# Kernel optimization log

Hardware: AMD Instinct MI355X
Metric: run time of the kernel (lower is better)

## Reference

```python
import jax, jax.numpy as jnp
import numpy as np
import math

VOCAB, D, L, B, S = 32000, 1024, 6, 4, 1024
FF = 4 * D


def sinusoidal_pe(max_len, d_model):
    pos = np.arange(max_len)[:, None].astype(np.float32)
    div = np.exp(np.arange(0, d_model, 2).astype(np.float32) * (-math.log(10000.0) / d_model))
    pe = np.zeros((max_len, d_model), dtype=np.float32)
    pe[:, 0::2] = np.sin(pos * div)
    pe[:, 1::2] = np.cos(pos * div)
    return jnp.asarray(pe)


def layernorm(x, g, b, eps=1e-5):
    mu = jnp.mean(x, axis=-1, keepdims=True)
    var = jnp.mean(jnp.square(x - mu), axis=-1, keepdims=True)
    return (x - mu) * jax.lax.rsqrt(var + eps) * g + b


def setup_inputs() -> dict:
    key = jax.random.key(0)
    ks = jax.random.split(key, 16)
    s = 0.02
    inp = {
        "input_ids": jax.random.randint(ks[0], (B, S), 0, VOCAB, dtype=jnp.int32),
        "attention_mask": jnp.ones((B, S), dtype=jnp.int32),
        "emb": jax.random.normal(ks[1], (VOCAB, D), jnp.float32) * s,
        "Wq": jax.random.normal(ks[2], (L, D, D), jnp.float32) * s,
        "Wk": jax.random.normal(ks[3], (L, D, D), jnp.float32) * s,
        "Wv": jax.random.normal(ks[4], (L, D, D), jnp.float32) * s,
        "bq": jnp.zeros((L, D), jnp.float32),
        "bk": jnp.zeros((L, D), jnp.float32),
        "bv": jnp.zeros((L, D), jnp.float32),
        "g1": jnp.ones((L, D), jnp.float32),
        "beta1": jnp.zeros((L, D), jnp.float32),
        "Wf1": jax.random.normal(ks[5], (L, D, FF), jnp.float32) * s,
        "bf1": jnp.zeros((L, FF), jnp.float32),
        "Wf2": jax.random.normal(ks[6], (L, FF, D), jnp.float32) * s,
        "bf2": jnp.zeros((L, D), jnp.float32),
        "g2": jnp.ones((L, D), jnp.float32),
        "beta2": jnp.zeros((L, D), jnp.float32),
    }
    return inp


def reference(input_ids, attention_mask, emb, Wq, Wk, Wv, bq, bk, bv,
              g1, beta1, Wf1, bf1, Wf2, bf2, g2, beta2):
    pe = sinusoidal_pe(1024, D)
    x = emb[input_ids] + pe[: input_ids.shape[1]]           # [B,S,D]
    mask = (attention_mask[:, None, :] != 0)                # [B,1,S]
    scale = 1.0 / math.sqrt(D)
    for l in range(L):
        Q = jnp.einsum('bsd,de->bse', x, Wq[l]) + bq[l]
        K = jnp.einsum('bsd,de->bse', x, Wk[l]) + bk[l]
        V = jnp.einsum('bsd,de->bse', x, Wv[l]) + bv[l]
        scores = jnp.einsum('bqd,bkd->bqk', Q, K) * scale   # [B,S,S]
        scores = jnp.where(mask, scores, -1e9)
        attn = jax.nn.softmax(scores, axis=-1)
        a = jnp.einsum('bqk,bkd->bqd', attn, V)
        x = layernorm(x + a, g1[l], beta1[l])
        h = jax.nn.relu(jnp.einsum('bsd,df->bsf', x, Wf1[l]) + bf1[l])
        f = jnp.einsum('bsf,fd->bsd', h, Wf2[l]) + bf2[l]
        x = layernorm(x + f, g2[l], beta2[l])
    return x
```

## Files before the change

### kernel.cpp

```cpp
#include <hip/hip_runtime.h>

typedef __bf16 bf16_t;
typedef __bf16 bf16x8 __attribute__((ext_vector_type(8)));
typedef float f32x4 __attribute__((ext_vector_type(4)));
typedef unsigned short u16;

#define DEV static __device__ __forceinline__

DEV float bf2f(u16 u) { __bf16 h = __builtin_bit_cast(__bf16, u); return (float)h; }
DEV u16 f2bf(float f) { __bf16 h = (__bf16)f; return __builtin_bit_cast(u16, h); }

DEV void gll16(bf16_t* lds, const bf16_t* g) {
    __builtin_amdgcn_global_load_lds(
        (const __attribute__((address_space(1))) void*)g,
        (__attribute__((address_space(3))) void*)lds, 16, 0, 0);
}

#define WAITV(N) asm volatile("s_waitcnt vmcnt(" #N ")" ::: "memory")

template <int EPI>
__global__ __launch_bounds__(512, 1)
void gemm8p(const bf16_t* __restrict__ A, int lda,
            const bf16_t* __restrict__ Bt, int ldb,
            bf16_t* __restrict__ C, int ldc,
            const float* __restrict__ bias, int K,
            long kadv, long cadv)
{
    __shared__ bf16_t Asm[2 * 2 * 8192];
    __shared__ bf16_t Bsm[2 * 2 * 8192];
    const int tid = threadIdx.x, w = tid >> 6, l = tid & 63;
    const int z = blockIdx.z;
    A  += (size_t)z * kadv;
    Bt += (size_t)z * kadv;
    C  += (size_t)z * cadv;

    const int gx = gridDim.x;
    int lin = blockIdx.y * gx + blockIdx.x;
    const int nlin = gx * gridDim.y;
    lin = (lin & 7) * (nlin >> 3) + (lin >> 3);
    const size_t row0 = (size_t)(lin / gx) * 256;
    const size_t col0 = (size_t)(lin % gx) * 256;

    const int wr = w >> 2, wc = w & 3;
    const int bh = wc >> 1;
    const int browoff = (wc & 1) * 64;
    const int fr = l & 15, q = l >> 4, sw = l & 7;

    const int srow = w * 8 + (l >> 3);
    const int sslot8 = ((l & 7) ^ ((l >> 3) & 7)) * 8;
    const bf16_t* AgH0 = A  + (row0 + srow) * (size_t)lda + sslot8;
    const bf16_t* BgH0 = Bt + (col0 + srow) * (size_t)ldb + sslot8;
    const size_t a128 = (size_t)128 * lda, b128 = (size_t)128 * ldb;
    const size_t a64  = (size_t)64 * lda,  b64  = (size_t)64 * ldb;
    const int wlds = w * 512;

#define STAGE_PAIR(buf, tt, p)                                                 \
    do {                                                                       \
        const int koff = (tt) * 64;                                            \
        if ((p) == 0) {                                                        \
            gll16(Asm + ((buf)*2+0)*8192 + wlds,        AgH0 + koff);          \
            gll16(Asm + ((buf)*2+0)*8192 + 4096 + wlds, AgH0 + koff + a64);    \
        } else if ((p) == 1) {                                                 \
            gll16(Asm + ((buf)*2+1)*8192 + wlds,        AgH0 + a128 + koff);   \
            gll16(Asm + ((buf)*2+1)*8192 + 4096 + wlds, AgH0 + a128 + koff + a64); \
        } else if ((p) == 2) {                                                 \
            gll16(Bsm + ((buf)*2+0)*8192 + wlds,        BgH0 + koff);          \
            gll16(Bsm + ((buf)*2+0)*8192 + 4096 + wlds, BgH0 + koff + b64);    \
        } else {                                                               \
            gll16(Bsm + ((buf)*2+1)*8192 + wlds,        BgH0 + b128 + koff);   \
            gll16(Bsm + ((buf)*2+1)*8192 + 4096 + wlds, BgH0 + b128 + koff + b64); \
        }                                                                      \
    } while (0)

    f32x4 acc[8][4] = {};
    const int NT = K >> 6;

    STAGE_PAIR(0, 0, 0); STAGE_PAIR(0, 0, 1); STAGE_PAIR(0, 0, 2); STAGE_PAIR(0, 0, 3);
    if (NT > 1) { STAGE_PAIR(1, 1, 0); WAITV(2); } else { WAITV(0); }
    __builtin_amdgcn_sched_barrier(0);
    __builtin_amdgcn_s_barrier();

    for (int t = 0; t < NT; ++t) {
        const int cur = t & 1, nxt = cur ^ 1;
        const bool hasN1 = (t + 1 < NT), hasN2 = (t + 2 < NT);
        const bf16_t* Ab = Asm + (cur * 2 + wr) * 8192;
        const bf16_t* Bb = Bsm + (cur * 2 + bh) * 8192;

        bf16x8 aR[4][2], bR[4][2];
#pragma unroll
        for (int mi = 0; mi < 4; mi++)
#pragma unroll
            for (int kk = 0; kk < 2; kk++)
                aR[mi][kk] = *(const bf16x8*)&Ab[(mi * 16 + fr) * 64 + ((kk * 4 + q) ^ sw) * 8];
#pragma unroll
        for (int ni = 0; ni < 4; ni++)
#pragma unroll
            for (int kk = 0; kk < 2; kk++)
                bR[ni][kk] = *(const bf16x8*)&Bb[(browoff + ni * 16 + fr) * 64 + ((kk * 4 + q) ^ sw) * 8];
        if (hasN1) { STAGE_PAIR(nxt, t + 1, 1); STAGE_PAIR(nxt, t + 1, 2); }
        __builtin_amdgcn_s_setprio(1);
#pragma unroll
        for (int mi = 0; mi < 4; mi++)
#pragma unroll
            for (int ni = 0; ni < 4; ni++)
#pragma unroll
                for (int kk = 0; kk < 2; kk++)
                    acc[mi][ni] = __builtin_amdgcn_mfma_f32_16x16x32_bf16(aR[mi][kk], bR[ni][kk], acc[mi][ni], 0, 0, 0);
        __builtin_amdgcn_s_setprio(0);

        bf16x8 a2[4][2];
#pragma unroll
        for (int mi = 0; mi < 4; mi++)
#pragma unroll
            for (int kk = 0; kk < 2; kk++)
                a2[mi][kk] = *(const bf16x8*)&Ab[((4 + mi) * 16 + fr) * 64 + ((kk * 4 + q) ^ sw) * 8];
        if (hasN1) STAGE_PAIR(nxt, t + 1, 3);
        __builtin_amdgcn_s_setprio(1);
#pragma unroll
        for (int mi = 0; mi < 4; mi++)
#pragma unroll
            for (int ni = 0; ni < 4; ni++)
#pragma unroll
                for (int kk = 0; kk < 2; kk++)
                    acc[4 + mi][ni] = __builtin_amdgcn_mfma_f32_16x16x32_bf16(a2[mi][kk], bR[ni][kk], acc[4 + mi][ni], 0, 0, 0);
        __builtin_amdgcn_s_setprio(0);

        __builtin_amdgcn_s_barrier();
        if (hasN2) STAGE_PAIR(cur, t + 2, 0);
        if (hasN1) {
            if (hasN2) { WAITV(2); } else { WAITV(0); }
            __builtin_amdgcn_sched_barrier(0);
        }
        __builtin_amdgcn_s_barrier();
    }
#undef STAGE_PAIR

    const int cr = q * 4, cc = fr;
#pragma unroll
    for (int ni = 0; ni < 4; ni++) {
        size_t c = col0 + wc * 64 + ni * 16 + cc;
        float bv = bias ? bias[c] : 0.f;
#pragma unroll
        for (int mi = 0; mi < 8; mi++) {
            size_t r = row0 + wr * 128 + mi * 16 + cr;
#pragma unroll
            for (int j = 0; j < 4; j++) {
                float v = acc[mi][ni][j] + bv;
                if (EPI == 1) v = fmaxf(v, 0.f);
                C[(r + j) * ldc + c] = (bf16_t)v;
            }
        }
    }
}

template <int EPI>
__global__ __launch_bounds__(256)
void gemm_db(const bf16_t* __restrict__ A, int lda, long sA,
             const bf16_t* __restrict__ Bt, int ldb, long sB,
             void* __restrict__ Cv, int ldc, long sC,
             const float* __restrict__ bias, int K, float scale)
{
    __shared__ bf16_t Asm[2][128 * 64];
    __shared__ bf16_t Bsm[2][128 * 64];
    const int tid = threadIdx.x, w = tid >> 6, l = tid & 63;
    const int bz = blockIdx.z;

    const int gx = gridDim.x;
    int lin = blockIdx.y * gx + blockIdx.x;
    const int nlin = gx * gridDim.y;
    lin = (lin & 7) * (nlin >> 3) + (lin >> 3);
    const size_t row0 = (size_t)(lin / gx) * 128;
    const size_t col0 = (size_t)(lin % gx) * 128;

    A  += (size_t)bz * sA;
    Bt += (size_t)bz * sB;

    const int lr = l >> 3;
    const int sl = (l & 7) ^ lr;
    const bf16_t* Ag = A  + (row0 + (size_t)(w * 32) + lr) * lda + sl * 8;
    const bf16_t* Bg = Bt + (col0 + (size_t)(w * 32) + lr) * ldb + sl * 8;
    const int wlds = (w * 32) * 64;

#define STA(buf, tt)                                                           \
    do { const int ko = (tt) * 64;                                             \
        _Pragma("unroll")                                                      \
        for (int c = 0; c < 4; c++)                                            \
            gll16(&Asm[buf][wlds + c * 8 * 64], Ag + (size_t)(c * 8) * lda + ko); \
    } while (0)
#define STB(buf, tt)                                                           \
    do { const int ko = (tt) * 64;                                             \
        _Pragma("unroll")                                                      \
        for (int c = 0; c < 4; c++)                                            \
            gll16(&Bsm[buf][wlds + c * 8 * 64], Bg + (size_t)(c * 8) * ldb + ko); \
    } while (0)

    const int wm = (w >> 1) * 64, wn = (w & 1) * 64;
    const int fr16 = l & 15, q4 = l >> 4, sw = l & 7;
    f32x4 acc[4][4] = {};
    const int NT = K >> 6;

    STA(0, 0); STB(0, 0);
    if (NT > 1) { STA(1, 1); WAITV(4); } else { WAITV(0); }
    __builtin_amdgcn_sched_barrier(0);
    __builtin_amdgcn_s_barrier();

    for (int t = 0; t < NT; ++t) {
        const int cur = t & 1, nxt = cur ^ 1;
        const bool hasN1 = (t + 1 < NT), hasN2 = (t + 2 < NT);

        bf16x8 a0[4], b0[4], a1[4], b1[4];
        const int s0 = (q4 ^ sw) * 8, s1 = ((4 + q4) ^ sw) * 8;
#pragma unroll
        for (int i = 0; i < 4; i++) {
            a0[i] = *(const bf16x8*)&Asm[cur][(wm + i * 16 + fr16) * 64 + s0];
            b0[i] = *(const bf16x8*)&Bsm[cur][(wn + i * 16 + fr16) * 64 + s0];
        }
        if (hasN1) STB(nxt, t + 1);
        __builtin_amdgcn_s_setprio(1);
#pragma unroll
        for (int mi = 0; mi < 4; mi++)
#pragma unroll
            for (int ni = 0; ni < 4; ni++)
                acc[mi][ni] = __builtin_amdgcn_mfma_f32_16x16x32_bf16(a0[mi], b0[ni], acc[mi][ni], 0, 0, 0);
        __builtin_amdgcn_s_setprio(0);
#pragma unroll
        for (int i = 0; i < 4; i++) {
            a1[i] = *(const bf16x8*)&Asm[cur][(wm + i * 16 + fr16) * 64 + s1];
            b1[i] = *(const bf16x8*)&Bsm[cur][(wn + i * 16 + fr16) * 64 + s1];
        }
        __builtin_amdgcn_s_setprio(1);
#pragma unroll
        for (int mi = 0; mi < 4; mi++)
#pragma unroll
            for (int ni = 0; ni < 4; ni++)
                acc[mi][ni] = __builtin_amdgcn_mfma_f32_16x16x32_bf16(a1[mi], b1[ni], acc[mi][ni], 0, 0, 0);
        __builtin_amdgcn_s_setprio(0);

        __builtin_amdgcn_s_barrier();
        if (hasN2) STA(cur, t + 2);
        if (hasN1) {
            if (hasN2) { WAITV(4); } else { WAITV(0); }
            __builtin_amdgcn_sched_barrier(0);
        }
        __builtin_amdgcn_s_barrier();
    }
#undef STA
#undef STB

    const int cr = q4 * 4, cc = fr16;
    if (EPI == 2) {
        float* C = (float*)Cv + (size_t)bz * sC;
#pragma unroll
        for (int mi = 0; mi < 4; mi++)
#pragma unroll
            for (int ni = 0; ni < 4; ni++) {
                size_t r = row0 + wm + mi * 16 + cr;
                size_t c = col0 + wn + ni * 16 + cc;
#pragma unroll
                for (int j = 0; j < 4; j++)
                    C[(r + j) * ldc + c] = acc[mi][ni][j] * scale;
            }
    } else if (EPI == 3) {
        bf16_t* C = (bf16_t*)Cv + (size_t)bz * sC;
#pragma unroll
        for (int mi = 0; mi < 4; mi++)
#pragma unroll
            for (int ni = 0; ni < 4; ni++) {
                size_t r = row0 + wm + mi * 16 + cr;
                size_t c = col0 + wn + ni * 16 + cc;
#pragma unroll
                for (int j = 0; j < 4; j++)
                    C[(r + j) * ldc + c] = (bf16_t)(acc[mi][ni][j] * scale);
            }
    } else {
        bf16_t* C = (bf16_t*)Cv + (size_t)bz * sC;
#pragma unroll
        for (int ni = 0; ni < 4; ni++) {
            size_t c = col0 + wn + ni * 16 + cc;
            float bv = bias ? bias[c] : 0.f;
#pragma unroll
            for (int mi = 0; mi < 4; mi++) {
                size_t r = row0 + wm + mi * 16 + cr;
#pragma unroll
                for (int j = 0; j < 4; j++) {
                    float v = acc[mi][ni][j] + bv;
                    if (EPI == 1) v = fmaxf(v, 0.f);
                    C[(r + j) * ldc + c] = (bf16_t)v;
                }
            }
        }
    }
}

__global__ __launch_bounds__(256)
void prep_kernel(const float* __restrict__ Wq, const float* __restrict__ Wk,
                 const float* __restrict__ Wv, const float* __restrict__ Wf1,
                 const float* __restrict__ Wf2,
                 const float* __restrict__ bq, const float* __restrict__ bk,
                 const float* __restrict__ bv,
                 const int* __restrict__ ids, const float* __restrict__ emb,
                 bf16_t* __restrict__ wqkvTA, bf16_t* __restrict__ wf1TA,
                 bf16_t* __restrict__ wf2TA, float* __restrict__ qbiasA,
                 float* __restrict__ x, bf16_t* __restrict__ xb)
{
    __shared__ bf16_t tls[64 * 64];
    const size_t DD = 1024 * 1024;
    int id = blockIdx.x;
    if (id < 16896) {
        const float* src; bf16_t* dst; int ldin, ldout, bx, by;
        if (id < 4608) {
            int layer = id / 768, r = id % 768, which = r >> 8, t = r & 255;
            src = (which == 0 ? Wq : which == 1 ? Wk : Wv) + (size_t)layer * DD;
            dst = wqkvTA + (size_t)layer * 3 * DD + (size_t)which * DD;
            ldin = 1024; ldout = 1024; bx = (t & 15) * 64; by = (t >> 4) * 64;
        } else if (id < 10752) {
            int i = id - 4608, layer = i >> 10, t = i & 1023;
            src = Wf1 + (size_t)layer * 4 * DD; dst = wf1TA + (size_t)layer * 4 * DD;
            ldin = 4096; ldout = 1024; bx = (t & 63) * 64; by = (t >> 6) * 64;
        } else {
            int i = id - 10752, layer = i >> 10, t = i & 1023;
            src = Wf2 + (size_t)layer * 4 * DD; dst = wf2TA + (size_t)layer * 4 * DD;
            ldin = 1024; ldout = 4096; bx = (t & 15) * 64; by = (t >> 4) * 64;
        }
        const int tid = threadIdx.x;
        const int cg = tid & 15, ri = tid >> 4;
#pragma unroll
        for (int k = 0; k < 4; k++) {
            int r = ri + k * 16;
            float4 v = *(const float4*)&src[(size_t)(by + r) * ldin + bx + cg * 4];
            ushort4 o = {f2bf(v.x), f2bf(v.y), f2bf(v.z), f2bf(v.w)};
            int g = cg ^ ((r >> 2) & 15);
            *(ushort4*)&tls[r * 64 + g * 4] = o;
        }
        __syncthreads();
#pragma unroll
        for (int k = 0; k < 4; k++) {
            int i2 = ri + k * 16;
            int gr = (i2 >> 2) ^ cg;
            ushort4 o;
            o.x = __builtin_bit_cast(u16, tls[(cg * 4 + 0) * 64 + gr * 4 + (i2 & 3)]);
            o.y = __builtin_bit_cast(u16, tls[(cg * 4 + 1) * 64 + gr * 4 + (i2 & 3)]);
            o.z = __builtin_bit_cast(u16, tls[(cg * 4 + 2) * 64 + gr * 4 + (i2 & 3)]);
            o.w = __builtin_bit_cast(u16, tls[(cg * 4 + 3) * 64 + gr * 4 + (i2 & 3)]);
            *(ushort4*)&dst[(size_t)(bx + i2) * ldout + by + cg * 4] = o;
        }
        return;
    }
    id -= 16896;
    if (id < 72) {
        int i = id * 256 + threadIdx.x;
        int lyr = i / 3072, j = i - lyr * 3072;
        qbiasA[i] = (j < 1024) ? bq[lyr * 1024 + j]
                  : (j < 2048) ? bk[lyr * 1024 + j - 1024]
                               : bv[lyr * 1024 + j - 2048];
        return;
    }
    id -= 72;
    const int row = id;
    const int s = row & 1023;
    const int eid = ids[row];
    const float* er = emb + (size_t)eid * 1024;
    float* xr = x + (size_t)row * 1024;
    bf16_t* br = xb + (size_t)row * 1024;
#pragma unroll
    for (int k = 0; k < 2; k++) {
        int i = threadIdx.x + 256 * k;
        int d = 2 * i;
        float dv = expf((float)d * -0.008994473019508f);
        float ph = (float)s * dv;
        float sv, cv;
        sincosf(ph, &sv, &cv);
        float2 ev = *(const float2*)&er[d];
        float x0 = ev.x + sv;
        float x1 = ev.y + cv;
        float2 xo = {x0, x1};
        *(float2*)&xr[d] = xo;
        ushort2 bo = {f2bf(x0), f2bf(x1)};
        *(ushort2*)&br[d] = bo;
    }
}

__global__ __launch_bounds__(256)
void softvt_kernel(const bf16_t* __restrict__ sc, const int* __restrict__ amask,
                   bf16_t* __restrict__ p, const bf16_t* __restrict__ qkv,
                   bf16_t* __restrict__ vt)
{
    __shared__ bf16_t tls[64][72];
    int bid = blockIdx.x;
    if (bid < 1024) {
        const int row = bid * 4 + (threadIdx.x >> 6);
        const int l = threadIdx.x & 63;
        const int b = row >> 10;
        const bf16_t* s = sc + (size_t)row * 1024;
        const int* m = amask + (size_t)b * 1024;
        float v[16];
        float mx = -3.0e38f;
#pragma unroll
        for (int i = 0; i < 4; i++) {
            int c = 4 * l + 256 * i;
            ushort4 su = *(const ushort4*)&s[c];
            int4 mv = *(const int4*)&m[c];
            v[4 * i + 0] = mv.x ? bf2f(su.x) : -1e9f;
            v[4 * i + 1] = mv.y ? bf2f(su.y) : -1e9f;
            v[4 * i + 2] = mv.z ? bf2f(su.z) : -1e9f;
            v[4 * i + 3] = mv.w ? bf2f(su.w) : -1e9f;
            mx = fmaxf(mx, fmaxf(fmaxf(v[4 * i], v[4 * i + 1]), fmaxf(v[4 * i + 2], v[4 * i + 3])));
        }
#pragma unroll
        for (int o = 32; o; o >>= 1) mx = fmaxf(mx, __shfl_xor(mx, o, 64));
        float sum = 0.f;
#pragma unroll
        for (int i = 0; i < 16; i++) { v[i] = __expf(v[i] - mx); sum += v[i]; }
#pragma unroll
        for (int o = 32; o; o >>= 1) sum += __shfl_xor(sum, o, 64);
        float inv = 1.0f / sum;
#pragma unroll
        for (int i = 0; i < 4; i++) {
            int c = 4 * l + 256 * i;
            ushort4 st;
            st.x = f2bf(v[4 * i + 0] * inv);
            st.y = f2bf(v[4 * i + 1] * inv);
            st.z = f2bf(v[4 * i + 2] * inv);
            st.w = f2bf(v[4 * i + 3] * inv);
            *(ushort4*)&p[(size_t)row * 1024 + c] = st;
        }
        return;
    }
    bid -= 1024;
    const int z = bid >> 8, t = bid & 255;
    const bf16_t* in = qkv + 2048 + (size_t)z * 1024 * 3072;
    bf16_t* out = vt + (size_t)z * 1024 * 1024;
    const int bx = (t & 15) * 64, by = (t >> 4) * 64;
    const int tid = threadIdx.x;
    const int cj = (tid & 15) * 4, ri = tid >> 4;
#pragma unroll
    for (int k = 0; k < 4; k++) {
        int r = ri + k * 16;
        *(ushort4*)&tls[r][cj] = *(const ushort4*)&in[(size_t)(by + r) * 3072 + bx + cj];
    }
    __syncthreads();
#pragma unroll
    for (int k = 0; k < 4; k++) {
        int i2 = ri + k * 16;
        ushort4 o;
        o.x = __builtin_bit_cast(u16, tls[cj + 0][i2]);
        o.y = __builtin_bit_cast(u16, tls[cj + 1][i2]);
        o.z = __builtin_bit_cast(u16, tls[cj + 2][i2]);
        o.w = __builtin_bit_cast(u16, tls[cj + 3][i2]);
        *(ushort4*)&out[(size_t)(bx + i2) * 1024 + by + cj] = o;
    }
}

__global__ __launch_bounds__(256)
void ln_kernel(const float* __restrict__ xin, const bf16_t* __restrict__ add,
               const float* __restrict__ g, const float* __restrict__ beta,
               float* __restrict__ xout, bf16_t* __restrict__ bout)
{
    __shared__ float red[8];
    const int row = blockIdx.x;
    const int t = threadIdx.x;
    const size_t base = (size_t)row * 1024 + t * 4;
    float4 xv = *(const float4*)&xin[base];
    ushort4 au = *(const ushort4*)&add[base];
    float tv[4];
    tv[0] = xv.x + bf2f(au.x);
    tv[1] = xv.y + bf2f(au.y);
    tv[2] = xv.z + bf2f(au.z);
    tv[3] = xv.w + bf2f(au.w);
    float s = tv[0] + tv[1] + tv[2] + tv[3];
    float s2 = tv[0] * tv[0] + tv[1] * tv[1] + tv[2] * tv[2] + tv[3] * tv[3];
#pragma unroll
    for (int o = 32; o; o >>= 1) { s += __shfl_xor(s, o, 64); s2 += __shfl_xor(s2, o, 64); }
    if ((t & 63) == 0) { red[t >> 6] = s; red[4 + (t >> 6)] = s2; }
    __syncthreads();
    s = red[0] + red[1] + red[2] + red[3];
    s2 = red[4] + red[5] + red[6] + red[7];
    const float mu = s * (1.f / 1024.f);
    const float var = s2 * (1.f / 1024.f) - mu * mu;
    const float rs = rsqrtf(var + 1e-5f);
    float4 gu = *(const float4*)&g[t * 4];
    float4 bu = *(const float4*)&beta[t * 4];
    float y0 = (tv[0] - mu) * rs * gu.x + bu.x;
    float y1 = (tv[1] - mu) * rs * gu.y + bu.y;
    float y2 = (tv[2] - mu) * rs * gu.z + bu.z;
    float y3 = (tv[3] - mu) * rs * gu.w + bu.w;
    float4 yo = {y0, y1, y2, y3};
    *(float4*)&xout[base] = yo;
    ushort4 ob = {f2bf(y0), f2bf(y1), f2bf(y2), f2bf(y3)};
    *(ushort4*)&bout[base] = ob;
}

__global__ __launch_bounds__(256)
void ln4_kernel(const float* __restrict__ xin, const bf16_t* __restrict__ p,
                long pstride, const float* __restrict__ fbias,
                const float* __restrict__ g, const float* __restrict__ beta,
                float* __restrict__ xout, bf16_t* __restrict__ bout)
{
    __shared__ float red[8];
    const int row = blockIdx.x;
    const int t = threadIdx.x;
    const size_t base = (size_t)row * 1024 + t * 4;
    float4 xv = *(const float4*)&xin[base];
    float4 bb = *(const float4*)&fbias[t * 4];
    float tv[4] = {xv.x + bb.x, xv.y + bb.y, xv.z + bb.z, xv.w + bb.w};
#pragma unroll
    for (int z = 0; z < 4; z++) {
        ushort4 au = *(const ushort4*)&p[(size_t)z * pstride + base];
        tv[0] += bf2f(au.x); tv[1] += bf2f(au.y);
        tv[2] += bf2f(au.z); tv[3] += bf2f(au.w);
    }
    float s = tv[0] + tv[1] + tv[2] + tv[3];
    float s2 = tv[0] * tv[0] + tv[1] * tv[1] + tv[2] * tv[2] + tv[3] * tv[3];
#pragma unroll
    for (int o = 32; o; o >>= 1) { s += __shfl_xor(s, o, 64); s2 += __shfl_xor(s2, o, 64); }
    if ((t & 63) == 0) { red[t >> 6] = s; red[4 + (t >> 6)] = s2; }
    __syncthreads();
    s = red[0] + red[1] + red[2] + red[3];
    s2 = red[4] + red[5] + red[6] + red[7];
    const float mu = s * (1.f / 1024.f);
    const float var = s2 * (1.f / 1024.f) - mu * mu;
    const float rs = rsqrtf(var + 1e-5f);
    float4 gu = *(const float4*)&g[t * 4];
    float4 bu = *(const float4*)&beta[t * 4];
    float y0 = (tv[0] - mu) * rs * gu.x + bu.x;
    float y1 = (tv[1] - mu) * rs * gu.y + bu.y;
    float y2 = (tv[2] - mu) * rs * gu.z + bu.z;
    float y3 = (tv[3] - mu) * rs * gu.w + bu.w;
    float4 yo = {y0, y1, y2, y3};
    *(float4*)&xout[base] = yo;
    ushort4 ob = {f2bf(y0), f2bf(y1), f2bf(y2), f2bf(y3)};
    *(ushort4*)&bout[base] = ob;
}


extern "C" void kernel_launch(void* const* d_in, const int* in_sizes, int n_in,
                              void* d_out, int out_size, void* d_ws, size_t ws_size,
                              hipStream_t stream)
{
    const int*   ids = (const int*)d_in[0];
    const int*   am  = (const int*)d_in[1];
    const float* emb = (const float*)d_in[2];
    const float* Wq  = (const float*)d_in[3];
    const float* Wk  = (const float*)d_in[4];
    const float* Wv  = (const float*)d_in[5];
    const float* bq  = (const float*)d_in[6];
    const float* bk  = (const float*)d_in[7];
    const float* bv  = (const float*)d_in[8];
    const float* g1  = (const float*)d_in[9];
    const float* be1 = (const float*)d_in[10];
    const float* Wf1 = (const float*)d_in[11];
    const float* bf1 = (const float*)d_in[12];
    const float* Wf2 = (const float*)d_in[13];
    const float* bf2_ = (const float*)d_in[14];
    const float* g2  = (const float*)d_in[15];
    const float* be2 = (const float*)d_in[16];

    char* ws = (char*)d_ws;
    float*  x      = (float*)(ws);
    bf16_t* xb     = (bf16_t*)(ws + (16LL << 20));
    bf16_t* qkv    = (bf16_t*)(ws + (24LL << 20));
    bf16_t* vt     = (bf16_t*)(ws + (48LL << 20));
    bf16_t* fpart  = (bf16_t*)(ws + (24LL << 20));
    bf16_t* scores = (bf16_t*)(ws + (56LL << 20));
    bf16_t* p      = (bf16_t*)(ws + (72LL << 20));
    bf16_t* h      = (bf16_t*)(ws + (56LL << 20));
    bf16_t* attn   = (bf16_t*)(ws + (88LL << 20));
    bf16_t* wqkvTA = (bf16_t*)(ws + (96LL << 20));
    bf16_t* wf1TA  = (bf16_t*)(ws + (132LL << 20));
    bf16_t* wf2TA  = (bf16_t*)(ws + (180LL << 20));
    float*  qbiasA = (float*)(ws + (228LL << 20));

    const size_t DD = 1024 * 1024;

    prep_kernel<<<21064, 256, 0, stream>>>(Wq, Wk, Wv, Wf1, Wf2, bq, bk, bv,
                                           ids, emb, wqkvTA, wf1TA, wf2TA, qbiasA, x, xb);

    for (int l = 0; l < 6; l++) {
        gemm8p<0><<<dim3(12, 16, 1), 512, 0, stream>>>(xb, 1024, wqkvTA + (size_t)l * 3 * DD, 1024,
                                                       qkv, 3072, qbiasA + l * 3072, 1024, 0, 0);
        gemm_db<3><<<dim3(8, 8, 4), 256, 0, stream>>>(qkv, 3072, 1024L * 3072,
                                                      qkv + 1024, 3072, 1024L * 3072,
                                                      scores, 1024, 1024L * 1024,
                                                      nullptr, 1024, 0.03125f);
        softvt_kernel<<<2048, 256, 0, stream>>>(scores, am, p, qkv, vt);
        gemm_db<0><<<dim3(8, 8, 4), 256, 0, stream>>>(p, 1024, 1024L * 1024,
                                                      vt, 1024, 1024L * 1024,
                                                      attn, 1024, 1024L * 1024,
                                                      nullptr, 1024, 0.f);
        ln_kernel<<<4096, 256, 0, stream>>>(x, attn, g1 + l * 1024, be1 + l * 1024, x, xb);
        gemm8p<1><<<dim3(16, 16, 1), 512, 0, stream>>>(xb, 1024, wf1TA + (size_t)l * 4 * DD, 1024,
                                                       h, 4096, bf1 + l * 4096, 1024, 0, 0);
        gemm8p<0><<<dim3(4, 16, 4), 512, 0, stream>>>(h, 4096, wf2TA + (size_t)l * 4 * DD, 4096,
                                                      fpart, 1024, nullptr, 1024,
                                                      1024, 4096L * 1024);
        float* xo = (l == 5) ? (float*)d_out : x;
        ln4_kernel<<<4096, 256, 0, stream>>>(x, fpart, 4096L * 1024, bf2_ + l * 1024,
                                             g2 + l * 1024, be2 + l * 1024, xo, xb);
    }
    (void)in_sizes; (void)n_in; (void)out_size; (void)ws_size;
}
```

Baseline: 1.262 ms.

## Stage whole GEMM tiles two iterations ahead instead of interleaved partial prefetch

Replaces the split prefetch scheme, where parts of the next K-tile were issued between MFMA phases, with staging each whole A and B tile two iterations ahead right after the barrier. Wait counts are adjusted so the next tile is resident. It simplifies the load schedule and gives each tile a full iteration of latency slack, but it drops the intra-iteration interleaving of loads with compute and bunches all global-to-LDS issues at one point.

```diff
diff --git a/kernel.cpp b/kernel.cpp
--- a/kernel.cpp
+++ b/kernel.cpp
@@ -54,34 +54,29 @@
     const size_t a64  = (size_t)64 * lda,  b64  = (size_t)64 * ldb;
     const int wlds = w * 512;
 
-#define STAGE_PAIR(buf, tt, p)                                                 \
+#define STAGE_TILE(buf, tt)                                                    \
     do {                                                                       \
         const int koff = (tt) * 64;                                            \
-        if ((p) == 0) {                                                        \
-            gll16(Asm + ((buf)*2+0)*8192 + wlds,        AgH0 + koff);          \
-            gll16(Asm + ((buf)*2+0)*8192 + 4096 + wlds, AgH0 + koff + a64);    \
-        } else if ((p) == 1) {                                                 \
-            gll16(Asm + ((buf)*2+1)*8192 + wlds,        AgH0 + a128 + koff);   \
-            gll16(Asm + ((buf)*2+1)*8192 + 4096 + wlds, AgH0 + a128 + koff + a64); \
-        } else if ((p) == 2) {                                                 \
-            gll16(Bsm + ((buf)*2+0)*8192 + wlds,        BgH0 + koff);          \
-            gll16(Bsm + ((buf)*2+0)*8192 + 4096 + wlds, BgH0 + koff + b64);    \
-        } else {                                                               \
-            gll16(Bsm + ((buf)*2+1)*8192 + wlds,        BgH0 + b128 + koff);   \
-            gll16(Bsm + ((buf)*2+1)*8192 + 4096 + wlds, BgH0 + b128 + koff + b64); \
-        }                                                                      \
+        gll16(Asm + ((buf)*2+0)*8192 + wlds,        AgH0 + koff);              \
+        gll16(Asm + ((buf)*2+0)*8192 + 4096 + wlds, AgH0 + koff + a64);        \
+        gll16(Asm + ((buf)*2+1)*8192 + wlds,        AgH0 + a128 + koff);       \
+        gll16(Asm + ((buf)*2+1)*8192 + 4096 + wlds, AgH0 + a128 + koff + a64); \
+        gll16(Bsm + ((buf)*2+0)*8192 + wlds,        BgH0 + koff);              \
+        gll16(Bsm + ((buf)*2+0)*8192 + 4096 + wlds, BgH0 + koff + b64);        \
+        gll16(Bsm + ((buf)*2+1)*8192 + wlds,        BgH0 + b128 + koff);       \
+        gll16(Bsm + ((buf)*2+1)*8192 + 4096 + wlds, BgH0 + b128 + koff + b64); \
     } while (0)
 
     f32x4 acc[8][4] = {};
     const int NT = K >> 6;
 
-    STAGE_PAIR(0, 0, 0); STAGE_PAIR(0, 0, 1); STAGE_PAIR(0, 0, 2); STAGE_PAIR(0, 0, 3);
-    if (NT > 1) { STAGE_PAIR(1, 1, 0); WAITV(2); } else { WAITV(0); }
+    STAGE_TILE(0, 0);
+    if (NT > 1) { STAGE_TILE(1, 1); WAITV(8); } else { WAITV(0); }
     __builtin_amdgcn_sched_barrier(0);
     __builtin_amdgcn_s_barrier();
 
     for (int t = 0; t < NT; ++t) {
-        const int cur = t & 1, nxt = cur ^ 1;
+        const int cur = t & 1;
         const bool hasN1 = (t + 1 < NT), hasN2 = (t + 2 < NT);
         const bf16_t* Ab = Asm + (cur * 2 + wr) * 8192;
         const bf16_t* Bb = Bsm + (cur * 2 + bh) * 8192;
@@ -97,7 +92,6 @@
 #pragma unroll
             for (int kk = 0; kk < 2; kk++)
                 bR[ni][kk] = *(const bf16x8*)&Bb[(browoff + ni * 16 + fr) * 64 + ((kk * 4 + q) ^ sw) * 8];
-        if (hasN1) { STAGE_PAIR(nxt, t + 1, 1); STAGE_PAIR(nxt, t + 1, 2); }
         __builtin_amdgcn_s_setprio(1);
 #pragma unroll
         for (int mi = 0; mi < 4; mi++)
@@ -114,7 +108,6 @@
 #pragma unroll
             for (int kk = 0; kk < 2; kk++)
                 a2[mi][kk] = *(const bf16x8*)&Ab[((4 + mi) * 16 + fr) * 64 + ((kk * 4 + q) ^ sw) * 8];
-        if (hasN1) STAGE_PAIR(nxt, t + 1, 3);
         __builtin_amdgcn_s_setprio(1);
 #pragma unroll
         for (int mi = 0; mi < 4; mi++)
@@ -126,14 +119,14 @@
         __builtin_amdgcn_s_setprio(0);
 
         __builtin_amdgcn_s_barrier();
-        if (hasN2) STAGE_PAIR(cur, t + 2, 0);
+        if (hasN2) STAGE_TILE(cur, t + 2);
         if (hasN1) {
-            if (hasN2) { WAITV(2); } else { WAITV(0); }
+            if (hasN2) { WAITV(8); } else { WAITV(0); }
             __builtin_amdgcn_sched_barrier(0);
         }
         __builtin_amdgcn_s_barrier();
     }
-#undef STAGE_PAIR
+#undef STAGE_TILE
 
     const int cr = q * 4, cc = fr;
 #pragma unroll
@@ -181,17 +174,13 @@
     const bf16_t* Bg = Bt + (col0 + (size_t)(w * 32) + lr) * ldb + sl * 8;
     const int wlds = (w * 32) * 64;
 
-#define STA(buf, tt)                                                           \
+#define STAGE_TILE(buf, tt)                                                    \
     do { const int ko = (tt) * 64;                                             \
         _Pragma("unroll")                                                      \
-        for (int c = 0; c < 4; c++)                                            \
+        for (int c = 0; c < 4; c++) {                                          \
             gll16(&Asm[buf][wlds + c * 8 * 64], Ag + (size_t)(c * 8) * lda + ko); \
-    } while (0)
-#define STB(buf, tt)                                                           \
-    do { const int ko = (tt) * 64;                                             \
-        _Pragma("unroll")                                                      \
-        for (int c = 0; c < 4; c++)                                            \
             gll16(&Bsm[buf][wlds + c * 8 * 64], Bg + (size_t)(c * 8) * ldb + ko); \
+        }                                                                      \
     } while (0)
 
     const int wm = (w >> 1) * 64, wn = (w & 1) * 64;
@@ -199,13 +188,13 @@
     f32x4 acc[4][4] = {};
     const int NT = K >> 6;
 
-    STA(0, 0); STB(0, 0);
-    if (NT > 1) { STA(1, 1); WAITV(4); } else { WAITV(0); }
+    STAGE_TILE(0, 0);
+    if (NT > 1) { STAGE_TILE(1, 1); WAITV(8); } else { WAITV(0); }
     __builtin_amdgcn_sched_barrier(0);
     __builtin_amdgcn_s_barrier();
 
     for (int t = 0; t < NT; ++t) {
-        const int cur = t & 1, nxt = cur ^ 1;
+        const int cur = t & 1;
         const bool hasN1 = (t + 1 < NT), hasN2 = (t + 2 < NT);
 
         bf16x8 a0[4], b0[4], a1[4], b1[4];
@@ -215,7 +204,6 @@
             a0[i] = *(const bf16x8*)&Asm[cur][(wm + i * 16 + fr16) * 64 + s0];
             b0[i] = *(const bf16x8*)&Bsm[cur][(wn + i * 16 + fr16) * 64 + s0];
         }
-        if (hasN1) STB(nxt, t + 1);
         __builtin_amdgcn_s_setprio(1);
 #pragma unroll
         for (int mi = 0; mi < 4; mi++)
@@ -237,15 +225,14 @@
         __builtin_amdgcn_s_setprio(0);
 
         __builtin_amdgcn_s_barrier();
-        if (hasN2) STA(cur, t + 2);
+        if (hasN2) STAGE_TILE(cur, t + 2);
         if (hasN1) {
-            if (hasN2) { WAITV(4); } else { WAITV(0); }
+            if (hasN2) { WAITV(8); } else { WAITV(0); }
             __builtin_amdgcn_sched_barrier(0);
         }
         __builtin_amdgcn_s_barrier();
     }
-#undef STA
-#undef STB
+#undef STAGE_TILE
 
     const int cr = q4 * 4, cc = fr16;
     if (EPI == 2) {
```

New measurement: 1.369 ms. 8.4% more time.
